# Performance work log

Hardware: AMD Instinct MI355X
Metric: run time of the kernel (lower is better)

## Reference

```python
import jax, jax.numpy as jnp
import numpy as np

EMBED_DIM = 1024
NUM_HEADS = 16
BATCH = 4
SEQ = 4096


def setup_inputs() -> dict:
    key = jax.random.key(0)
    ks = jax.random.split(key, 5)
    scale = 0.02
    E = EMBED_DIM
    x = jax.random.normal(ks[0], (BATCH, SEQ, E), dtype=jnp.float32)
    Wq = jax.random.normal(ks[1], (E, E), dtype=jnp.float32) * scale
    Wk = jax.random.normal(ks[2], (E, E), dtype=jnp.float32) * scale
    Wv = jax.random.normal(ks[3], (E, E), dtype=jnp.float32) * scale
    Wo = jax.random.normal(ks[4], (E, E), dtype=jnp.float32) * scale
    z = jnp.zeros((E,), dtype=jnp.float32)
    return {"x": x, "Wq": Wq, "bq": z, "Wk": Wk, "bk": z, "Wv": Wv, "bv": z, "Wo": Wo, "bo": z}


def reference(x, Wq, bq, Wk, bk, Wv, bv, Wo, bo):
    B, S, E = x.shape
    H = NUM_HEADS
    D = E // H
    # torch nn.Linear: y = x @ W.T + b
    def proj(W, b):
        return (jnp.einsum('bse,fe->bsf', x, W) + b).reshape(B, S, H, D)
    q = jax.nn.elu(proj(Wq, bq)) + 1.0  # [B,S,H,D] feature map
    k = jax.nn.elu(proj(Wk, bk)) + 1.0
    v = proj(Wv, bv)
    # kv aggregation over sequence: [B,H,D,D]
    kv = jnp.einsum('bshd,bshe->bhde', k, v)
    # Q . KV: [B,S,H,D] -> merge heads -> [B,S,E]
    out = jnp.einsum('bshd,bhde->bshe', q, kv).reshape(B, S, E)
    # output projection (dropout is identity at inference)
    out = jnp.einsum('bse,fe->bsf', out, Wo) + bo
    return out
```

## Files before the change

### kernel.cpp

```cpp
#include <hip/hip_runtime.h>
#include <hip/hip_bf16.h>
#include <cstdint>
#include <cstddef>

#define BATCH 4
#define SEQ   4096
#define EMB   1024
#define NH    16
#define HD    64
#define M_TOT (BATCH * SEQ)
#define KV_CHUNKS 16

using bf16_t = __hip_bfloat16;
typedef __attribute__((ext_vector_type(8))) short bv8;
typedef __attribute__((ext_vector_type(4))) float f32x4;

union SV8 { bv8 v; bf16_t h[8]; };

__device__ __forceinline__ void gload_lds16(const void* g, void* l) {
  __builtin_amdgcn_global_load_lds(
      (const __attribute__((address_space(1))) unsigned int*)g,
      (__attribute__((address_space(3))) unsigned int*)l, 16, 0, 0);
}

__global__ __launch_bounds__(256) void cvt_kernel(const float* __restrict__ in,
                                                  bf16_t* __restrict__ out) {
  const size_t i = ((size_t)blockIdx.x * 256 + threadIdx.x) * 8;
  const f32x4 a = *(const f32x4*)(in + i);
  const f32x4 b = *(const f32x4*)(in + i + 4);
  SV8 o;
#pragma unroll
  for (int j = 0; j < 4; ++j) o.h[j] = __float2bfloat16(a[j]);
#pragma unroll
  for (int j = 0; j < 4; ++j) o.h[4 + j] = __float2bfloat16(b[j]);
  *(bv8*)(out + i) = o.v;
}

template <bool QKV>
__global__ __launch_bounds__(512, 2) void gemm256(
    const bf16_t* __restrict__ A, const bf16_t* __restrict__ W,
    const float* __restrict__ b0, const float* __restrict__ b1,
    const float* __restrict__ b2, void* __restrict__ o0,
    void* __restrict__ o1, void* __restrict__ o2) {
  constexpr int K = 1024;
  constexpr int NT = QKV ? 12 : 4;
  constexpr int NKT = K / 32;
  __shared__ char lds[131072];

  const int nwg = NT * 64;
  const int wg = (blockIdx.x & 7) * (nwg >> 3) + (blockIdx.x >> 3);
  const int m0 = (wg / NT) * 256;
  const int n0 = (wg % NT) * 256;
  const int t = threadIdx.x, l = t & 63, w = t >> 6;
  const int wm = w >> 2, wn = w & 3;

  const int s0r = (t >> 6) * 16 + (t & 15), s0c = ((t >> 4) & 3) * 8;
  const int s1 = 512 + t;
  const int s1r = (s1 >> 6) * 16 + (s1 & 15), s1c = ((s1 >> 4) & 3) * 8;
  const bf16_t* a0 = A + (size_t)(m0 + s0r) * K + s0c;
  const bf16_t* a1 = A + (size_t)(m0 + s1r) * K + s1c;
  const bf16_t* w0 = W + (size_t)(n0 + s0r) * K + s0c;
  const bf16_t* w1 = W + (size_t)(n0 + s1r) * K + s1c;
  char* la0 = lds + t * 16;
  char* la1 = lds + 8192 + t * 16;
  char* lb0 = lds + 65536 + t * 16;
  char* lb1 = lds + 65536 + 8192 + t * 16;

  f32x4 acc[8][4] = {};

  auto STAGE = [&](int tile, int q) {
    const size_t ko = (size_t)tile * 32;
    const int qo = q * 16384;
    gload_lds16(a0 + ko, la0 + qo);
    gload_lds16(w0 + ko, lb0 + qo);
    gload_lds16(a1 + ko, la1 + qo);
    gload_lds16(w1 + ko, lb1 + qo);
  };
  auto COMPUTE = [&](int q) {
    const char* ab = lds + q * 16384 + wm * 8192 + l * 16;
    const char* bb = lds + 65536 + q * 16384 + wn * 4096 + l * 16;
    bv8 af[8], bf[4];
#pragma unroll
    for (int m = 0; m < 8; ++m) af[m] = *(const bv8*)(ab + m * 1024);
#pragma unroll
    for (int n = 0; n < 4; ++n) bf[n] = *(const bv8*)(bb + n * 1024);
#pragma unroll
    for (int m = 0; m < 8; ++m)
#pragma unroll
      for (int n = 0; n < 4; ++n)
        acc[m][n] = __builtin_amdgcn_mfma_f32_16x16x32_bf16(af[m], bf[n],
                                                            acc[m][n], 0, 0, 0);
  };

  STAGE(0, 0);
  STAGE(1, 1);
  STAGE(2, 2);
  asm volatile("s_waitcnt vmcnt(8)" ::: "memory");
  __builtin_amdgcn_s_barrier();

  for (int kt = 0; kt < NKT - 3; ++kt) {
    STAGE(kt + 3, (kt + 3) & 3);
    COMPUTE(kt & 3);
    asm volatile("s_waitcnt vmcnt(8)" ::: "memory");
    __builtin_amdgcn_s_barrier();
  }
  COMPUTE((NKT - 3) & 3);
  asm volatile("s_waitcnt vmcnt(4)" ::: "memory");
  __builtin_amdgcn_s_barrier();
  COMPUTE((NKT - 2) & 3);
  asm volatile("s_waitcnt vmcnt(0)" ::: "memory");
  __builtin_amdgcn_s_barrier();
  COMPUTE((NKT - 1) & 3);

  const int gq = n0 >> 10;
  const float* bias = QKV ? (gq == 0 ? b0 : (gq == 1 ? b1 : b2)) : b0;
  bf16_t* ob = (bf16_t*)(gq == 0 ? o0 : (gq == 1 ? o1 : o2));
  const int cb = (n0 & 1023) + wn * 64;
  const int rb = m0 + wm * 128 + ((l >> 4) << 2);
  const int cc = l & 15;
#pragma unroll
  for (int n = 0; n < 4; ++n) {
    const int col = cb + n * 16 + cc;
    const float bz = bias[col];
#pragma unroll
    for (int m = 0; m < 8; ++m) {
      const int row = rb + m * 16;
#pragma unroll
      for (int r = 0; r < 4; ++r) {
        float v = acc[m][n][r] + bz;
        if (QKV) {
          if (gq < 2) v = (v > 0.f) ? (v + 1.f) : __expf(v);
          ob[(size_t)(row + r) * 1024 + col] = __float2bfloat16(v);
        } else {
          ((float*)o0)[(size_t)(row + r) * 1024 + col] = v;
        }
      }
    }
  }
}

__global__ __launch_bounds__(256) void kv_partial(const bf16_t* __restrict__ Kmat,
                                                  const bf16_t* __restrict__ Vmat,
                                                  float* __restrict__ pkv) {
  const int chunk = blockIdx.x;
  const int bh = blockIdx.y;
  const int b = bh >> 4, h = bh & 15;
  const int t = threadIdx.x;
  __shared__ bf16_t kl[8][64], vl[8][64];
  float acc[16] = {};
  const int e = t & 63, d0 = (t >> 6) * 16;
  const int sl = t >> 5, c2 = (t & 31) * 2;
  const int s0 = chunk * (SEQ / KV_CHUNKS);
  const bf16_t* kp = Kmat + ((size_t)(b * SEQ + s0 + sl)) * EMB + h * 64 + c2;
  const bf16_t* vp = Vmat + ((size_t)(b * SEQ + s0 + sl)) * EMB + h * 64 + c2;
  for (int it = 0; it < (SEQ / KV_CHUNKS) / 8; ++it) {
    const unsigned int kw = *(const unsigned int*)kp;
    const unsigned int vw = *(const unsigned int*)vp;
    __syncthreads();
    *(unsigned int*)&kl[sl][c2] = kw;
    *(unsigned int*)&vl[sl][c2] = vw;
    __syncthreads();
#pragma unroll
    for (int ss = 0; ss < 8; ++ss) {
      const float vv = __bfloat162float(vl[ss][e]);
      SV8 k0, k1;
      k0.v = *(const bv8*)&kl[ss][d0];
      k1.v = *(const bv8*)&kl[ss][d0 + 8];
#pragma unroll
      for (int dd = 0; dd < 8; ++dd) acc[dd] += __bfloat162float(k0.h[dd]) * vv;
#pragma unroll
      for (int dd = 0; dd < 8; ++dd) acc[8 + dd] += __bfloat162float(k1.h[dd]) * vv;
    }
    kp += 8 * EMB;
    vp += 8 * EMB;
  }
  float* outp = pkv + ((size_t)chunk * 64 + bh) * 4096;
#pragma unroll
  for (int dd = 0; dd < 16; ++dd) outp[(d0 + dd) * 64 + e] = acc[dd];
}

__global__ __launch_bounds__(256) void kv_reduce(const float* __restrict__ pkv,
                                                 bf16_t* __restrict__ kvT) {
  const int bh = blockIdx.x;
  const int t = threadIdx.x;
  __shared__ float tile[64][65];
#pragma unroll
  for (int ii = 0; ii < 16; ++ii) {
    const int idx = ii * 256 + t;
    float s = 0.f;
#pragma unroll
    for (int c = 0; c < KV_CHUNKS; ++c)
      s += pkv[((size_t)c * 64 + bh) * 4096 + idx];
    tile[idx >> 6][idx & 63] = s;
  }
  __syncthreads();
  bf16_t* outp = kvT + (size_t)bh * 4096;
#pragma unroll
  for (int ii = 0; ii < 16; ++ii) {
    const int o = ii * 256 + t;
    outp[o] = __float2bfloat16(tile[o & 63][o >> 6]);
  }
}

__global__ __launch_bounds__(256, 4) void qkv_apply(const bf16_t* __restrict__ Q,
                                                    const bf16_t* __restrict__ kvT,
                                                    bf16_t* __restrict__ ctx) {
  __shared__ bf16_t Ql[128 * 64];
  __shared__ bf16_t Bl[64 * 64];
  const int st = blockIdx.x;
  const int bh = blockIdx.y;
  const int b = bh >> 4, h = bh & 15;
  const int t = threadIdx.x, l = t & 63, w = t >> 6;

  const size_t qbase = ((size_t)(b * SEQ + st * 128)) * EMB + h * 64;
#pragma unroll
  for (int j = 0; j < 4; ++j) {
    const int vt = j * 256 + t;
    const int fb = vt >> 6;
    const int row = (fb >> 1) * 16 + (vt & 15);
    const int col = (fb & 1) * 32 + (((vt >> 4) & 3) << 3);
    gload_lds16(Q + qbase + (size_t)row * EMB + col, (char*)Ql + vt * 16);
  }
  const bf16_t* kvb = kvT + (size_t)bh * 4096;
#pragma unroll
  for (int j = 0; j < 2; ++j) {
    const int vt = j * 256 + t;
    const int fb = vt >> 6;
    const int row = (fb >> 1) * 16 + (vt & 15);
    const int col = (fb & 1) * 32 + (((vt >> 4) & 3) << 3);
    gload_lds16(kvb + row * 64 + col, (char*)Bl + vt * 16);
  }
  __syncthreads();

  f32x4 acc[2][4] = {};
#pragma unroll
  for (int kt = 0; kt < 2; ++kt) {
    bv8 a[2], bb[4];
#pragma unroll
    for (int i = 0; i < 2; ++i)
      a[i] = *(const bv8*)((const char*)Ql + (((w * 2 + i) * 2 + kt) * 1024) + l * 16);
#pragma unroll
    for (int j = 0; j < 4; ++j)
      bb[j] = *(const bv8*)((const char*)Bl + ((j * 2 + kt) * 1024) + l * 16);
#pragma unroll
    for (int i = 0; i < 2; ++i)
#pragma unroll
      for (int j = 0; j < 4; ++j)
        acc[i][j] = __builtin_amdgcn_mfma_f32_16x16x32_bf16(a[i], bb[j],
                                                            acc[i][j], 0, 0, 0);
  }

  const int cr = (l >> 4) << 2, cc = l & 15;
#pragma unroll
  for (int i = 0; i < 2; ++i)
#pragma unroll
    for (int j = 0; j < 4; ++j)
#pragma unroll
      for (int r = 0; r < 4; ++r) {
        const int row = st * 128 + w * 32 + i * 16 + cr + r;
        ctx[((size_t)(b * SEQ + row)) * EMB + h * 64 + j * 16 + cc] =
            __float2bfloat16(acc[i][j][r]);
      }
}

extern "C" void kernel_launch(void* const* d_in, const int* in_sizes, int n_in,
                              void* d_out, int out_size, void* d_ws, size_t ws_size,
                              hipStream_t stream) {
  (void)in_sizes; (void)n_in; (void)out_size;
  const float* x  = (const float*)d_in[0];
  const float* Wq = (const float*)d_in[1];
  const float* bq = (const float*)d_in[2];
  const float* Wk = (const float*)d_in[3];
  const float* bk = (const float*)d_in[4];
  const float* Wv = (const float*)d_in[5];
  const float* bv = (const float*)d_in[6];
  const float* Wo = (const float*)d_in[7];
  const float* bo = (const float*)d_in[8];

  const size_t NEED = 33554432ull + 4ull * 2097152ull + 33554432ull +
                      16777216ull + 524288ull;
  if (ws_size < NEED) return;

  char* p = (char*)d_ws;
  bf16_t* xb   = (bf16_t*)p;
  bf16_t* wqkv = (bf16_t*)(p + 33554432ull);
  bf16_t* wob  = (bf16_t*)(p + 33554432ull + 3ull * 2097152ull);
  bf16_t* vbuf = (bf16_t*)(p + 33554432ull + 4ull * 2097152ull);
  float*  pkv  = (float*)(p + 2ull * 33554432ull + 4ull * 2097152ull);
  bf16_t* kvT  = (bf16_t*)(p + 2ull * 33554432ull + 4ull * 2097152ull + 16777216ull);
  bf16_t* ctx  = xb;

  bf16_t* qb = (bf16_t*)d_out;
  bf16_t* kb = qb + (size_t)M_TOT * EMB;

  cvt_kernel<<<8192, 256, 0, stream>>>(x, xb);
  cvt_kernel<<<512, 256, 0, stream>>>(Wq, wqkv);
  cvt_kernel<<<512, 256, 0, stream>>>(Wk, wqkv + 1024 * 1024);
  cvt_kernel<<<512, 256, 0, stream>>>(Wv, wqkv + 2048 * 1024);
  cvt_kernel<<<512, 256, 0, stream>>>(Wo, wob);

  gemm256<true><<<768, 512, 0, stream>>>(xb, wqkv, bq, bk, bv, qb, kb, vbuf);

  kv_partial<<<dim3(KV_CHUNKS, 64), 256, 0, stream>>>(kb, vbuf, pkv);
  kv_reduce<<<64, 256, 0, stream>>>(pkv, kvT);

  qkv_apply<<<dim3(32, 64), 256, 0, stream>>>(qb, kvT, ctx);

  gemm256<false><<<256, 512, 0, stream>>>(ctx, wob, bo, nullptr, nullptr,
                                          d_out, nullptr, nullptr);
}
```

Measured before the change: 408.8 us.

## Fold KV into output projection and rewrite GEMM with 8-phase pipelined schedule

Folds the per-head KV matrices into Wo, building a per-batch matrix M_b = blockdiag(kv)·Wo^T. The final GEMM then consumes Q directly, and the qkv_apply pass that wrote a full context tensor is removed. The GEMM is rewritten to use K-tiles of 64 with double buffering and a phase-interleaved load/MFMA schedule using s_setprio. The four weight conversions are merged into one launch, and the workspace layout is reorganised. This adds a small fold kernel and an extra bf16 rounding of the folded matrix, which changes numerics slightly.

```diff
diff --git a/kernel.cpp b/kernel.cpp
--- a/kernel.cpp
+++ b/kernel.cpp
@@ -6,8 +6,6 @@
 #define BATCH 4
 #define SEQ   4096
 #define EMB   1024
-#define NH    16
-#define HD    64
 #define M_TOT (BATCH * SEQ)
 #define KV_CHUNKS 16
 
@@ -22,6 +20,8 @@
       (const __attribute__((address_space(1))) unsigned int*)g,
       (__attribute__((address_space(3))) unsigned int*)l, 16, 0, 0);
 }
+
+#define BAR() asm volatile("s_barrier" ::: "memory")
 
 __global__ __launch_bounds__(256) void cvt_kernel(const float* __restrict__ in,
                                                   bf16_t* __restrict__ out) {
@@ -36,104 +36,183 @@
   *(bv8*)(out + i) = o.v;
 }
 
-template <bool QKV>
-__global__ __launch_bounds__(512, 2) void gemm256(
-    const bf16_t* __restrict__ A, const bf16_t* __restrict__ W,
+__global__ __launch_bounds__(256) void wcvt_kernel(
+    const float* __restrict__ s0, const float* __restrict__ s1,
+    const float* __restrict__ s2, const float* __restrict__ s3,
+    bf16_t* __restrict__ d0, bf16_t* __restrict__ d1,
+    bf16_t* __restrict__ d2, bf16_t* __restrict__ d3) {
+  const float* in; bf16_t* out;
+  switch (blockIdx.y) {
+    case 0:  in = s0; out = d0; break;
+    case 1:  in = s1; out = d1; break;
+    case 2:  in = s2; out = d2; break;
+    default: in = s3; out = d3; break;
+  }
+  const size_t i = ((size_t)blockIdx.x * 256 + threadIdx.x) * 8;
+  const f32x4 a = *(const f32x4*)(in + i);
+  const f32x4 b = *(const f32x4*)(in + i + 4);
+  SV8 o;
+#pragma unroll
+  for (int j = 0; j < 4; ++j) o.h[j] = __float2bfloat16(a[j]);
+#pragma unroll
+  for (int j = 0; j < 4; ++j) o.h[4 + j] = __float2bfloat16(b[j]);
+  *(bv8*)(out + i) = o.v;
+}
+
+template <int VARIANT>
+__global__ __launch_bounds__(512, 2) void gemm8p(
+    const bf16_t* __restrict__ A, const bf16_t* __restrict__ Wbase,
     const float* __restrict__ b0, const float* __restrict__ b1,
     const float* __restrict__ b2, void* __restrict__ o0,
     void* __restrict__ o1, void* __restrict__ o2) {
   constexpr int K = 1024;
-  constexpr int NT = QKV ? 12 : 4;
-  constexpr int NKT = K / 32;
+  constexpr int NT = (VARIANT == 0) ? 12 : 4;
+  constexpr int NKT = K / 64;
   __shared__ char lds[131072];
 
   const int nwg = NT * 64;
   const int wg = (blockIdx.x & 7) * (nwg >> 3) + (blockIdx.x >> 3);
   const int m0 = (wg / NT) * 256;
   const int n0 = (wg % NT) * 256;
+  const bf16_t* W = Wbase + (VARIANT ? (size_t)(m0 >> 12) * 1048576ull : 0);
   const int t = threadIdx.x, l = t & 63, w = t >> 6;
   const int wm = w >> 2, wn = w & 3;
 
-  const int s0r = (t >> 6) * 16 + (t & 15), s0c = ((t >> 4) & 3) * 8;
-  const int s1 = 512 + t;
-  const int s1r = (s1 >> 6) * 16 + (s1 & 15), s1c = ((s1 >> 4) & 3) * 8;
-  const bf16_t* a0 = A + (size_t)(m0 + s0r) * K + s0c;
-  const bf16_t* a1 = A + (size_t)(m0 + s1r) * K + s1c;
-  const bf16_t* w0 = W + (size_t)(n0 + s0r) * K + s0c;
-  const bf16_t* w1 = W + (size_t)(n0 + s1r) * K + s1c;
-  char* la0 = lds + t * 16;
-  char* la1 = lds + 8192 + t * 16;
-  char* lb0 = lds + 65536 + t * 16;
-  char* lb1 = lds + 65536 + 8192 + t * 16;
+  const int sr = ((t >> 7) << 4) + (t & 15);
+  const int sc = (((t >> 6) & 1) << 5) + (((t >> 4) & 3) << 3);
+  const bf16_t* aRow = A + (size_t)(m0 + sr) * K + sc;
+  const bf16_t* wRow = W + (size_t)(n0 + sr) * K + sc;
+  char* dA = lds + t * 16;
+  char* dB = lds + 65536 + t * 16;
+
+  auto ST = [&](int isB, int hf, int kt) {
+    char* d = (isB ? dB : dA) + (kt & 1) * 32768 + hf * 16384;
+    const bf16_t* s = (isB ? wRow : aRow) + (size_t)(hf * 128) * K + kt * 64;
+    gload_lds16(s, d);
+    gload_lds16(s + (size_t)64 * K, d + 8192);
+  };
+
+  const char* Ab = lds + wm * 16384 + l * 16;
+  const char* Bb = lds + 65536 + (wn >> 1) * 16384 + (wn & 1) * 8192 + l * 16;
 
   f32x4 acc[8][4] = {};
-
-  auto STAGE = [&](int tile, int q) {
-    const size_t ko = (size_t)tile * 32;
-    const int qo = q * 16384;
-    gload_lds16(a0 + ko, la0 + qo);
-    gload_lds16(w0 + ko, lb0 + qo);
-    gload_lds16(a1 + ko, la1 + qo);
-    gload_lds16(w1 + ko, lb1 + qo);
-  };
-  auto COMPUTE = [&](int q) {
-    const char* ab = lds + q * 16384 + wm * 8192 + l * 16;
-    const char* bb = lds + 65536 + q * 16384 + wn * 4096 + l * 16;
-    bv8 af[8], bf[4];
-#pragma unroll
-    for (int m = 0; m < 8; ++m) af[m] = *(const bv8*)(ab + m * 1024);
-#pragma unroll
-    for (int n = 0; n < 4; ++n) bf[n] = *(const bv8*)(bb + n * 1024);
-#pragma unroll
-    for (int m = 0; m < 8; ++m)
-#pragma unroll
-      for (int n = 0; n < 4; ++n)
-        acc[m][n] = __builtin_amdgcn_mfma_f32_16x16x32_bf16(af[m], bf[n],
-                                                            acc[m][n], 0, 0, 0);
-  };
-
-  STAGE(0, 0);
-  STAGE(1, 1);
-  STAGE(2, 2);
-  asm volatile("s_waitcnt vmcnt(8)" ::: "memory");
-  __builtin_amdgcn_s_barrier();
-
-  for (int kt = 0; kt < NKT - 3; ++kt) {
-    STAGE(kt + 3, (kt + 3) & 3);
-    COMPUTE(kt & 3);
-    asm volatile("s_waitcnt vmcnt(8)" ::: "memory");
-    __builtin_amdgcn_s_barrier();
-  }
-  COMPUTE((NKT - 3) & 3);
-  asm volatile("s_waitcnt vmcnt(4)" ::: "memory");
-  __builtin_amdgcn_s_barrier();
-  COMPUTE((NKT - 2) & 3);
-  asm volatile("s_waitcnt vmcnt(0)" ::: "memory");
-  __builtin_amdgcn_s_barrier();
-  COMPUTE((NKT - 1) & 3);
-
-  const int gq = n0 >> 10;
-  const float* bias = QKV ? (gq == 0 ? b0 : (gq == 1 ? b1 : b2)) : b0;
-  bf16_t* ob = (bf16_t*)(gq == 0 ? o0 : (gq == 1 ? o1 : o2));
-  const int cb = (n0 & 1023) + wn * 64;
-  const int rb = m0 + wm * 128 + ((l >> 4) << 2);
-  const int cc = l & 15;
-#pragma unroll
-  for (int n = 0; n < 4; ++n) {
-    const int col = cb + n * 16 + cc;
-    const float bz = bias[col];
-#pragma unroll
-    for (int m = 0; m < 8; ++m) {
-      const int row = rb + m * 16;
-#pragma unroll
-      for (int r = 0; r < 4; ++r) {
-        float v = acc[m][n][r] + bz;
-        if (QKV) {
+  bv8 af[4][2], bf[4][2];
+
+  ST(1, 0, 0); ST(1, 1, 0); ST(0, 0, 0); ST(0, 1, 0);
+  ST(1, 0, 1); ST(1, 1, 1); ST(0, 0, 1);
+  asm volatile("s_waitcnt vmcnt(6)" ::: "memory");
+  BAR();
+
+#pragma unroll 1
+  for (int j = 0; j < NKT; ++j) {
+    const int db = (j & 1) * 32768;
+#pragma unroll
+    for (int mb = 0; mb < 4; ++mb)
+#pragma unroll
+      for (int ks = 0; ks < 2; ++ks)
+        af[mb][ks] = *(const bv8*)(Ab + db + mb * 2048 + ks * 1024);
+#pragma unroll
+    for (int nb = 0; nb < 4; ++nb)
+#pragma unroll
+      for (int ks = 0; ks < 2; ++ks)
+        bf[nb][ks] = *(const bv8*)(Bb + db + nb * 2048 + ks * 1024);
+    if (j + 1 < NKT) ST(0, 1, j + 1);
+    BAR();
+    __builtin_amdgcn_s_setprio(1);
+#pragma unroll
+    for (int mb = 0; mb < 4; ++mb)
+#pragma unroll
+      for (int nb = 0; nb < 2; ++nb)
+#pragma unroll
+        for (int ks = 0; ks < 2; ++ks)
+          acc[mb][nb] = __builtin_amdgcn_mfma_f32_16x16x32_bf16(
+              af[mb][ks], bf[nb][ks], acc[mb][nb], 0, 0, 0);
+    __builtin_amdgcn_s_setprio(0);
+    BAR();
+    if (j + 2 < NKT) ST(1, 0, j + 2);
+    BAR();
+    __builtin_amdgcn_s_setprio(1);
+#pragma unroll
+    for (int mb = 0; mb < 4; ++mb)
+#pragma unroll
+      for (int nb = 2; nb < 4; ++nb)
+#pragma unroll
+        for (int ks = 0; ks < 2; ++ks)
+          acc[mb][nb] = __builtin_amdgcn_mfma_f32_16x16x32_bf16(
+              af[mb][ks], bf[nb][ks], acc[mb][nb], 0, 0, 0);
+    __builtin_amdgcn_s_setprio(0);
+    BAR();
+#pragma unroll
+    for (int mb = 0; mb < 4; ++mb)
+#pragma unroll
+      for (int ks = 0; ks < 2; ++ks)
+        af[mb][ks] = *(const bv8*)(Ab + db + 8192 + mb * 2048 + ks * 1024);
+    if (j + 2 < NKT) ST(1, 1, j + 2);
+    BAR();
+    __builtin_amdgcn_s_setprio(1);
+#pragma unroll
+    for (int mb = 0; mb < 4; ++mb)
+#pragma unroll
+      for (int nb = 2; nb < 4; ++nb)
+#pragma unroll
+        for (int ks = 0; ks < 2; ++ks)
+          acc[4 + mb][nb] = __builtin_amdgcn_mfma_f32_16x16x32_bf16(
+              af[mb][ks], bf[nb][ks], acc[4 + mb][nb], 0, 0, 0);
+    __builtin_amdgcn_s_setprio(0);
+    BAR();
+    if (j + 2 < NKT) {
+      ST(0, 0, j + 2);
+      asm volatile("s_waitcnt vmcnt(6)" ::: "memory");
+    } else if (j == NKT - 2) {
+      asm volatile("s_waitcnt vmcnt(0)" ::: "memory");
+    }
+    BAR();
+    __builtin_amdgcn_s_setprio(1);
+#pragma unroll
+    for (int mb = 0; mb < 4; ++mb)
+#pragma unroll
+      for (int nb = 0; nb < 2; ++nb)
+#pragma unroll
+        for (int ks = 0; ks < 2; ++ks)
+          acc[4 + mb][nb] = __builtin_amdgcn_mfma_f32_16x16x32_bf16(
+              af[mb][ks], bf[nb][ks], acc[4 + mb][nb], 0, 0, 0);
+    __builtin_amdgcn_s_setprio(0);
+    BAR();
+  }
+
+  const int cr = (l >> 4) << 2, cc = l & 15;
+  if (VARIANT == 0) {
+    const int gq = n0 >> 10;
+    const float* bias = gq == 0 ? b0 : (gq == 1 ? b1 : b2);
+    bf16_t* ob = (bf16_t*)(gq == 0 ? o0 : (gq == 1 ? o1 : o2));
+    const int cb = (n0 & 1023) + wn * 64;
+#pragma unroll
+    for (int nb = 0; nb < 4; ++nb) {
+      const int col = cb + nb * 16 + cc;
+      const float bz = bias[col];
+#pragma unroll
+      for (int mb = 0; mb < 8; ++mb) {
+        const int row = m0 + wm * 128 + mb * 16 + cr;
+#pragma unroll
+        for (int r = 0; r < 4; ++r) {
+          float v = acc[mb][nb][r] + bz;
           if (gq < 2) v = (v > 0.f) ? (v + 1.f) : __expf(v);
           ob[(size_t)(row + r) * 1024 + col] = __float2bfloat16(v);
-        } else {
-          ((float*)o0)[(size_t)(row + r) * 1024 + col] = v;
         }
+      }
+    }
+  } else {
+    const int cb = n0 + wn * 64;
+#pragma unroll
+    for (int nb = 0; nb < 4; ++nb) {
+      const int col = cb + nb * 16 + cc;
+      const float bz = b0[col];
+#pragma unroll
+      for (int mb = 0; mb < 8; ++mb) {
+        const int row = m0 + wm * 128 + mb * 16 + cr;
+#pragma unroll
+        for (int r = 0; r < 4; ++r)
+          ((float*)o0)[(size_t)(row + r) * 1024 + col] = acc[mb][nb][r] + bz;
       }
     }
   }
@@ -180,10 +259,9 @@
 }
 
 __global__ __launch_bounds__(256) void kv_reduce(const float* __restrict__ pkv,
-                                                 bf16_t* __restrict__ kvT) {
+                                                 bf16_t* __restrict__ kvf) {
   const int bh = blockIdx.x;
   const int t = threadIdx.x;
-  __shared__ float tile[64][65];
 #pragma unroll
   for (int ii = 0; ii < 16; ++ii) {
     const int idx = ii * 256 + t;
@@ -191,76 +269,61 @@
 #pragma unroll
     for (int c = 0; c < KV_CHUNKS; ++c)
       s += pkv[((size_t)c * 64 + bh) * 4096 + idx];
-    tile[idx >> 6][idx & 63] = s;
-  }
-  __syncthreads();
-  bf16_t* outp = kvT + (size_t)bh * 4096;
-#pragma unroll
-  for (int ii = 0; ii < 16; ++ii) {
-    const int o = ii * 256 + t;
-    outp[o] = __float2bfloat16(tile[o & 63][o >> 6]);
-  }
-}
-
-__global__ __launch_bounds__(256, 4) void qkv_apply(const bf16_t* __restrict__ Q,
-                                                    const bf16_t* __restrict__ kvT,
-                                                    bf16_t* __restrict__ ctx) {
-  __shared__ bf16_t Ql[128 * 64];
-  __shared__ bf16_t Bl[64 * 64];
-  const int st = blockIdx.x;
+    kvf[(size_t)bh * 4096 + idx] = __float2bfloat16(s);
+  }
+}
+
+__global__ __launch_bounds__(256) void fold_kernel(const bf16_t* __restrict__ Wo,
+                                                   const bf16_t* __restrict__ kvf,
+                                                   bf16_t* __restrict__ MT) {
+  __shared__ char lds[24576];
+  const int ft = blockIdx.x;
   const int bh = blockIdx.y;
   const int b = bh >> 4, h = bh & 15;
   const int t = threadIdx.x, l = t & 63, w = t >> 6;
-
-  const size_t qbase = ((size_t)(b * SEQ + st * 128)) * EMB + h * 64;
-#pragma unroll
-  for (int j = 0; j < 4; ++j) {
-    const int vt = j * 256 + t;
-    const int fb = vt >> 6;
-    const int row = (fb >> 1) * 16 + (vt & 15);
-    const int col = (fb & 1) * 32 + (((vt >> 4) & 3) << 3);
-    gload_lds16(Q + qbase + (size_t)row * EMB + col, (char*)Ql + vt * 16);
-  }
-  const bf16_t* kvb = kvT + (size_t)bh * 4096;
-#pragma unroll
-  for (int j = 0; j < 2; ++j) {
-    const int vt = j * 256 + t;
-    const int fb = vt >> 6;
-    const int row = (fb >> 1) * 16 + (vt & 15);
-    const int col = (fb & 1) * 32 + (((vt >> 4) & 3) << 3);
-    gload_lds16(kvb + row * 64 + col, (char*)Bl + vt * 16);
-  }
-  __syncthreads();
-
+#pragma unroll
+  for (int q = 0; q < 4; ++q) {
+    const int s = q * 256 + t;
+    const int row = ((s >> 7) << 4) + (s & 15);
+    const int col = (((s >> 6) & 1) << 5) + (((s >> 4) & 3) << 3);
+    gload_lds16(Wo + (size_t)(ft * 128 + row) * 1024 + h * 64 + col, lds + s * 16);
+  }
+#pragma unroll
+  for (int q = 0; q < 2; ++q) {
+    const int s = q * 256 + t;
+    const int row = ((s >> 7) << 4) + (s & 15);
+    const int col = (((s >> 6) & 1) << 5) + (((s >> 4) & 3) << 3);
+    gload_lds16(kvf + (size_t)bh * 4096 + row * 64 + col, lds + 16384 + s * 16);
+  }
+  asm volatile("s_waitcnt vmcnt(0)" ::: "memory");
+  BAR();
   f32x4 acc[2][4] = {};
 #pragma unroll
-  for (int kt = 0; kt < 2; ++kt) {
-    bv8 a[2], bb[4];
+  for (int ks = 0; ks < 2; ++ks) {
+    bv8 am[2], bn[4];
 #pragma unroll
     for (int i = 0; i < 2; ++i)
-      a[i] = *(const bv8*)((const char*)Ql + (((w * 2 + i) * 2 + kt) * 1024) + l * 16);
-#pragma unroll
-    for (int j = 0; j < 4; ++j)
-      bb[j] = *(const bv8*)((const char*)Bl + ((j * 2 + kt) * 1024) + l * 16);
+      am[i] = *(const bv8*)(lds + (w * 2 + i) * 2048 + ks * 1024 + l * 16);
+#pragma unroll
+    for (int nb = 0; nb < 4; ++nb)
+      bn[nb] = *(const bv8*)(lds + 16384 + nb * 2048 + ks * 1024 + l * 16);
 #pragma unroll
     for (int i = 0; i < 2; ++i)
 #pragma unroll
-      for (int j = 0; j < 4; ++j)
-        acc[i][j] = __builtin_amdgcn_mfma_f32_16x16x32_bf16(a[i], bb[j],
-                                                            acc[i][j], 0, 0, 0);
-  }
-
+      for (int nb = 0; nb < 4; ++nb)
+        acc[i][nb] = __builtin_amdgcn_mfma_f32_16x16x32_bf16(am[i], bn[nb],
+                                                             acc[i][nb], 0, 0, 0);
+  }
+  bf16_t* out = MT + (size_t)b * 1048576ull;
   const int cr = (l >> 4) << 2, cc = l & 15;
 #pragma unroll
   for (int i = 0; i < 2; ++i)
 #pragma unroll
-    for (int j = 0; j < 4; ++j)
-#pragma unroll
-      for (int r = 0; r < 4; ++r) {
-        const int row = st * 128 + w * 32 + i * 16 + cr + r;
-        ctx[((size_t)(b * SEQ + row)) * EMB + h * 64 + j * 16 + cc] =
-            __float2bfloat16(acc[i][j][r]);
-      }
+    for (int nb = 0; nb < 4; ++nb)
+#pragma unroll
+      for (int r = 0; r < 4; ++r)
+        out[(size_t)(ft * 128 + w * 32 + i * 16 + cr + r) * 1024 + h * 64 +
+            nb * 16 + cc] = __float2bfloat16(acc[i][nb][r]);
 }
 
 extern "C" void kernel_launch(void* const* d_in, const int* in_sizes, int n_in,
@@ -277,35 +340,31 @@
   const float* Wo = (const float*)d_in[7];
   const float* bo = (const float*)d_in[8];
 
-  const size_t NEED = 33554432ull + 4ull * 2097152ull + 33554432ull +
-                      16777216ull + 524288ull;
+  const size_t NEED = 72ull * 1024 * 1024;
   if (ws_size < NEED) return;
 
   char* p = (char*)d_ws;
   bf16_t* xb   = (bf16_t*)p;
+  float*  pkv  = (float*)p;
+  bf16_t* kvf  = (bf16_t*)(p + 16777216ull);
+  bf16_t* MT   = (bf16_t*)(p + 17825792ull);
   bf16_t* wqkv = (bf16_t*)(p + 33554432ull);
-  bf16_t* wob  = (bf16_t*)(p + 33554432ull + 3ull * 2097152ull);
-  bf16_t* vbuf = (bf16_t*)(p + 33554432ull + 4ull * 2097152ull);
-  float*  pkv  = (float*)(p + 2ull * 33554432ull + 4ull * 2097152ull);
-  bf16_t* kvT  = (bf16_t*)(p + 2ull * 33554432ull + 4ull * 2097152ull + 16777216ull);
-  bf16_t* ctx  = xb;
-
-  bf16_t* qb = (bf16_t*)d_out;
-  bf16_t* kb = qb + (size_t)M_TOT * EMB;
+  bf16_t* wob  = (bf16_t*)(p + 39845888ull);
+  bf16_t* qb   = (bf16_t*)(p + 41943040ull);
+
+  bf16_t* kb = (bf16_t*)d_out;
+  bf16_t* vb = kb + 16777216ull;
 
   cvt_kernel<<<8192, 256, 0, stream>>>(x, xb);
-  cvt_kernel<<<512, 256, 0, stream>>>(Wq, wqkv);
-  cvt_kernel<<<512, 256, 0, stream>>>(Wk, wqkv + 1024 * 1024);
-  cvt_kernel<<<512, 256, 0, stream>>>(Wv, wqkv + 2048 * 1024);
-  cvt_kernel<<<512, 256, 0, stream>>>(Wo, wob);
-
-  gemm256<true><<<768, 512, 0, stream>>>(xb, wqkv, bq, bk, bv, qb, kb, vbuf);
-
-  kv_partial<<<dim3(KV_CHUNKS, 64), 256, 0, stream>>>(kb, vbuf, pkv);
-  kv_reduce<<<64, 256, 0, stream>>>(pkv, kvT);
-
-  qkv_apply<<<dim3(32, 64), 256, 0, stream>>>(qb, kvT, ctx);
-
-  gemm256<false><<<256, 512, 0, stream>>>(ctx, wob, bo, nullptr, nullptr,
-                                          d_out, nullptr, nullptr);
-}
+  wcvt_kernel<<<dim3(512, 4), 256, 0, stream>>>(
+      Wq, Wk, Wv, Wo, wqkv, wqkv + 1048576, wqkv + 2097152, wob);
+
+  gemm8p<0><<<768, 512, 0, stream>>>(xb, wqkv, bq, bk, bv, qb, kb, vb);
+
+  kv_partial<<<dim3(KV_CHUNKS, 64), 256, 0, stream>>>(kb, vb, pkv);
+  kv_reduce<<<64, 256, 0, stream>>>(pkv, kvf);
+  fold_kernel<<<dim3(8, 64), 256, 0, stream>>>(wob, kvf, MT);
+
+  gemm8p<1><<<256, 512, 0, stream>>>(qb, MT, bo, nullptr, nullptr,
+                                     d_out, nullptr, nullptr);
+}
```

Result: faster. 389.7 us (-4.7%).
